# Kernel tuning notes

Hardware: AMD Instinct MI355X
Metric: run time of the kernel (lower is better)

The kernel has to match this reference:

```python
import jax, jax.numpy as jnp
import numpy as np

HEADS = 16
D_MODEL = 1024
D_HEAD = D_MODEL // HEADS


def setup_inputs() -> dict:
    key = jax.random.key(0)
    ks = jax.random.split(key, 12)
    B, S = 4, 2048
    scale = D_MODEL ** -0.5
    inp = {
        "q": jax.random.normal(ks[0], (B, S, D_MODEL), jnp.float32),
        "k": jax.random.normal(ks[1], (B, S, D_MODEL), jnp.float32),
        "v": jax.random.normal(ks[2], (B, S, D_MODEL), jnp.float32),
        # causal mask: True = masked position
        "mask": jnp.triu(jnp.ones((S, S), bool), k=1)[None].repeat(B, axis=0),
        "wq": jax.random.normal(ks[3], (D_MODEL, D_MODEL), jnp.float32) * scale,
        "bq": jnp.zeros((D_MODEL,), jnp.float32),
        "wk": jax.random.normal(ks[4], (D_MODEL, D_MODEL), jnp.float32) * scale,
        "bk": jnp.zeros((D_MODEL,), jnp.float32),
        "wv": jax.random.normal(ks[5], (D_MODEL, D_MODEL), jnp.float32) * scale,
        "bv": jnp.zeros((D_MODEL,), jnp.float32),
        "wo": jax.random.normal(ks[6], (D_MODEL, D_MODEL), jnp.float32) * scale,
        "bo": jnp.zeros((D_MODEL,), jnp.float32),
    }
    return inp


def _split_head(x):
    B, S, _ = x.shape
    return x.reshape(B, S, HEADS, D_HEAD).transpose(0, 2, 1, 3)  # [B,H,S,D]


def reference(q, k, v, mask, wq, bq, wk, bk, wv, bv, wo, bo):
    # linear projections (torch Linear: x @ W^T + b)
    qh = _split_head(q @ wq.T + bq) * (D_HEAD ** -0.5)
    kh = _split_head(k @ wk.T + bk)
    vh = _split_head(v @ wv.T + bv)
    # scores [B,H,Sq,Sk]
    scores = jnp.einsum("bhqd,bhkd->bhqk", qh, kh)
    scores = jnp.where(mask[:, None, :, :], -1e20, scores)
    weights = jax.nn.softmax(scores, axis=-1)  # dropout p=0 in eval
    ctx = jnp.einsum("bhqk,bhkd->bhqd", weights, vh)
    B, H, S, D = ctx.shape
    ctx = ctx.transpose(0, 2, 1, 3).reshape(B, S, H * D)
    return ctx @ wo.T + bo
```

## Files before the change

kernel.cpp:

```cpp
#include <hip/hip_runtime.h>
#include <hip/hip_bf16.h>
#include <cstdint>
#include <cstddef>

typedef unsigned short u16;
typedef unsigned int u32;
using short8  = __attribute__((ext_vector_type(8))) short;
using f32x4   = __attribute__((ext_vector_type(4))) float;
using f32x16  = __attribute__((ext_vector_type(16))) float;
using u32x4   = __attribute__((ext_vector_type(4))) u32;

#define SCALE_Q 0.18033688011112043f

#define WAITVM(N) asm volatile("s_waitcnt vmcnt(" #N ")" ::: "memory")

__device__ inline u16 f2bf(float f) {
  return __builtin_bit_cast(u16, __float2bfloat16(f));
}

__device__ inline u32 cvt_pk_bf16(float a, float b) {
  u32 r;
  asm("v_cvt_pk_bf16_f32 %0, %1, %2" : "=v"(r) : "v"(a), "v"(b));
  return r;
}

__device__ inline f32x4 mfma16(short8 a, short8 b, f32x4 c) {
  return __builtin_amdgcn_mfma_f32_16x16x32_bf16(a, b, c, 0, 0, 0);
}
__device__ inline f32x16 mfma32(short8 a, short8 b, f32x16 c) {
  return __builtin_amdgcn_mfma_f32_32x32x16_bf16(a, b, c, 0, 0, 0);
}

__device__ inline void gload16(const void* g, void* l) {
  __builtin_amdgcn_global_load_lds(
      (const __attribute__((address_space(1))) void*)g,
      (__attribute__((address_space(3))) void*)l,
      16, 0, 0);
}

__global__ __launch_bounds__(256)
void prep(const float* __restrict__ q, const float* __restrict__ k,
          const float* __restrict__ v,
          const float* __restrict__ wq, const float* __restrict__ wk,
          const float* __restrict__ wv, const float* __restrict__ wo,
          u16* __restrict__ Wb, u16* __restrict__ Act) {
  const int c = blockIdx.x * 256 + threadIdx.x;
  const float* src;
  u16* dst;
  float sc = 1.f;
  size_t off;
  if (c < 524288) {
    const int m = c >> 17;
    off = (size_t)(c & 131071) * 8;
    src = (m == 0) ? wq : (m == 1) ? wk : (m == 2) ? wv : wo;
    if (m == 0) sc = SCALE_Q;
    dst = Wb + (size_t)m * 1048576;
  } else {
    const int c2 = c - 524288;
    const int m = c2 >> 20;
    off = (size_t)(c2 & 1048575) * 8;
    src = (m == 0) ? q : (m == 1) ? k : v;
    dst = Act + (size_t)m * 8388608;
  }
  f32x4 a = *(const f32x4*)(src + off);
  f32x4 b = *(const f32x4*)(src + off + 4);
  short8 vv;
#pragma unroll
  for (int j = 0; j < 4; ++j) { vv[j] = (short)f2bf(a[j] * sc); vv[4 + j] = (short)f2bf(b[j] * sc); }
  *(short8*)&dst[off] = vv;
}

struct GemmArgs {
  const u16* Act; const u16* ctx; const u16* Wb;
  const float* bq; const float* bk; const float* bv; const float* bo;
  u16* Qs; u16* Ks; u16* Vs; float* out;
};

__global__ __launch_bounds__(256, 3)
void gemm_proj(GemmArgs ga, int modeBase) {
  const int mode = modeBase + blockIdx.z;
  const int bx = blockIdx.x;
  const int bm = ((bx & 7) << 3) | (bx >> 3);
  const int bn = blockIdx.y;
  const int tid = threadIdx.x;
  const int w = tid >> 6, lane = tid & 63;
  const int wr = w >> 1, wc = w & 1;
  const int l15 = lane & 15, g = lane >> 4;

  const u16* Am = (mode == 3) ? ga.ctx : ga.Act + (size_t)mode * 8388608;
  const u16* Wm = ga.Wb + (size_t)mode * 1048576;
  const float* bias = (mode == 0) ? ga.bq : (mode == 1) ? ga.bk : (mode == 2) ? ga.bv : ga.bo;

  __shared__ u16 As[2][128 * 64];
  __shared__ u16 Bs[2][128 * 64];

  f32x4 acc[4][4] = {};
  const int m0 = bm * 128, n0 = bn * 128;

  const int r_lo = lane >> 3;
  const int sc8 = ((lane & 7) ^ (lane >> 3)) * 8;

  auto stage = [&](int k0, int slot) {
#pragma unroll
    for (int i = 0; i < 4; ++i) {
      const int row = i * 32 + w * 8 + r_lo;
      const int db = i * 2048 + w * 512;
      gload16(Am + (size_t)(m0 + row) * 1024 + k0 + sc8, &As[slot][db]);
      gload16(Wm + (size_t)(n0 + row) * 1024 + k0 + sc8, &Bs[slot][db]);
    }
  };

  auto compute = [&](int slot) {
#pragma unroll
    for (int kk = 0; kk < 2; ++kk) {
      short8 av[4], bv4[4];
#pragma unroll
      for (int mi = 0; mi < 4; ++mi) {
        const int row = wr * 64 + mi * 16 + l15;
        av[mi] = *(const short8*)&As[slot][row * 64 + ((((kk << 2) | g)) ^ (row & 7)) * 8];
      }
#pragma unroll
      for (int ni = 0; ni < 4; ++ni) {
        const int row = wc * 64 + ni * 16 + l15;
        bv4[ni] = *(const short8*)&Bs[slot][row * 64 + ((((kk << 2) | g)) ^ (row & 7)) * 8];
      }
#pragma unroll
      for (int mi = 0; mi < 4; ++mi)
#pragma unroll
        for (int ni = 0; ni < 4; ++ni)
          acc[mi][ni] = mfma16(av[mi], bv4[ni], acc[mi][ni]);
    }
  };

  stage(0, 0);
  stage(64, 1);

#pragma unroll 2
  for (int t = 0; t < 14; ++t) {
    WAITVM(8);
    __builtin_amdgcn_s_barrier();
    __builtin_amdgcn_sched_barrier(0);
    compute(t & 1);
    __builtin_amdgcn_s_barrier();
    __builtin_amdgcn_sched_barrier(0);
    stage((t + 2) * 64, t & 1);
  }
  WAITVM(8);
  __builtin_amdgcn_s_barrier();
  __builtin_amdgcn_sched_barrier(0);
  compute(0);
  WAITVM(0);
  __builtin_amdgcn_s_barrier();
  __builtin_amdgcn_sched_barrier(0);
  compute(1);

  float bvals[4];
#pragma unroll
  for (int ni = 0; ni < 4; ++ni)
    bvals[ni] = bias[n0 + wc * 64 + ni * 16 + l15] * ((mode == 0) ? SCALE_Q : 1.f);

  if (mode == 3) {
#pragma unroll
    for (int mi = 0; mi < 4; ++mi)
#pragma unroll
      for (int ni = 0; ni < 4; ++ni)
#pragma unroll
        for (int r = 0; r < 4; ++r) {
          const int m = m0 + wr * 64 + mi * 16 + g * 4 + r;
          const int n = n0 + wc * 64 + ni * 16 + l15;
          ga.out[(size_t)m * 1024 + n] = acc[mi][ni][r] + bvals[ni];
        }
  } else {
    u16* O = (mode == 0) ? ga.Qs : (mode == 1) ? ga.Ks : ga.Vs;
#pragma unroll
    for (int mi = 0; mi < 4; ++mi)
#pragma unroll
      for (int ni = 0; ni < 4; ++ni)
#pragma unroll
        for (int r = 0; r < 4; ++r) {
          const int m = m0 + wr * 64 + mi * 16 + g * 4 + r;
          const int n = n0 + wc * 64 + ni * 16 + l15;
          const int b = m >> 11, s = m & 2047, hh = n >> 6, d = n & 63;
          const float val = acc[mi][ni][r] + bvals[ni];
          const size_t base = (size_t)(b * 16 + hh) * 131072;
          size_t idx;
          if (mode == 2) {
            const int sp = (s & ~12) | ((s & 4) << 1) | ((s & 8) >> 1);
            const int kt = sp >> 5, w5 = sp & 31;
            const int j = ((d >> 5) << 1) | (w5 >> 4);
            const int hi2 = (w5 >> 3) & 1, e = w5 & 7;
            idx = base + (size_t)kt * 2048 + j * 512 + hi2 * 256 + (d & 31) * 8 + e;
          } else {
            const int s32 = s >> 5, l31 = s & 31;
            const int t2 = d >> 4, hi2 = (d >> 3) & 1, e = d & 7;
            idx = base + (size_t)s32 * 2048 + t2 * 512 + hi2 * 256 + l31 * 8 + e;
          }
          O[idx] = f2bf(val);
        }
  }
}

__global__ __launch_bounds__(256)
void attn_fwd(const u16* __restrict__ Qs, const u16* __restrict__ Ks,
              const u16* __restrict__ Vs, u16* __restrict__ ctx) {
  const int bh = blockIdx.x;
  const int qt = 15 - blockIdx.y;
  const int tid = threadIdx.x;
  const int w = tid >> 6, lane = tid & 63;
  const int l31 = lane & 31, hi = lane >> 5;

  const u16* Qb = Qs + (size_t)bh * 131072;
  const u16* Kb = Ks + (size_t)bh * 131072 + lane * 8;
  const u16* Vb = Vs + (size_t)bh * 131072 + lane * 8;
  const int b = bh >> 4, hh = bh & 15;

  const int qw0 = qt * 128 + w * 32;
  const int nkt = (qw0 >> 5) + 1;
  const int qrow = qw0 + l31;

  short8 qf[4];
  {
    const u16* qp = Qb + (size_t)(qw0 >> 5) * 2048 + lane * 8;
#pragma unroll
    for (int t = 0; t < 4; ++t) qf[t] = *(const short8*)(qp + t * 512);
  }

  f32x16 oacc0 = {}, oacc1 = {};
  float lsum = 0.f;

  auto body = [&](const short8* kf, const short8* vf, int kt, bool last) {
    f32x16 st = {};
    __builtin_amdgcn_s_setprio(1);
    st = mfma32(kf[0], qf[0], st);
    st = mfma32(kf[1], qf[1], st);
    st = mfma32(kf[2], qf[2], st);
    st = mfma32(kf[3], qf[3], st);
    __builtin_amdgcn_s_setprio(0);
    if (last) {
#pragma unroll
      for (int r = 0; r < 16; ++r) {
        const int ka = kt * 32 + (r & 3) + 8 * (r >> 2) + 4 * hi;
        if (ka > qrow) st[r] = -1e30f;
      }
    }
    float p[16];
#pragma unroll
    for (int r = 0; r < 16; ++r) p[r] = __builtin_amdgcn_exp2f(st[r]);
    {
      float s0 = (p[0] + p[1]) + (p[2] + p[3]);
      float s1 = (p[4] + p[5]) + (p[6] + p[7]);
      float s2 = (p[8] + p[9]) + (p[10] + p[11]);
      float s3 = (p[12] + p[13]) + (p[14] + p[15]);
      lsum += (s0 + s1) + (s2 + s3);
    }
    u32x4 a0, a1;
#pragma unroll
    for (int v2 = 0; v2 < 4; ++v2) {
      a0[v2] = cvt_pk_bf16(p[2 * v2], p[2 * v2 + 1]);
      a1[v2] = cvt_pk_bf16(p[8 + 2 * v2], p[9 + 2 * v2]);
    }
    const short8 pb0 = __builtin_bit_cast(short8, a0);
    const short8 pb1 = __builtin_bit_cast(short8, a1);
    __builtin_amdgcn_s_setprio(1);
    oacc0 = mfma32(vf[0], pb0, oacc0);
    oacc0 = mfma32(vf[1], pb1, oacc0);
    oacc1 = mfma32(vf[2], pb0, oacc1);
    oacc1 = mfma32(vf[3], pb1, oacc1);
    __builtin_amdgcn_s_setprio(0);
  };

  short8 kA[4], vA[4], kB[4], vB[4];
#pragma unroll
  for (int t = 0; t < 4; ++t) {
    kA[t] = *(const short8*)(Kb + t * 512);
    vA[t] = *(const short8*)(Vb + t * 512);
  }

  for (int kt = 0; ; ) {
    const bool lastA = (kt + 1 == nkt);
    if (!lastA) {
      const u16* kp = Kb + (size_t)(kt + 1) * 2048;
      const u16* vp = Vb + (size_t)(kt + 1) * 2048;
#pragma unroll
      for (int t = 0; t < 4; ++t) {
        kB[t] = *(const short8*)(kp + t * 512);
        vB[t] = *(const short8*)(vp + t * 512);
      }
    }
    body(kA, vA, kt, lastA);
    if (lastA) break;
    ++kt;
    const bool lastB = (kt + 1 == nkt);
    if (!lastB) {
      const u16* kp = Kb + (size_t)(kt + 1) * 2048;
      const u16* vp = Vb + (size_t)(kt + 1) * 2048;
#pragma unroll
      for (int t = 0; t < 4; ++t) {
        kA[t] = *(const short8*)(kp + t * 512);
        vA[t] = *(const short8*)(vp + t * 512);
      }
    }
    body(kB, vB, kt, lastB);
    if (lastB) break;
    ++kt;
  }

  lsum += __shfl_xor(lsum, 32);
  const float inv = __builtin_amdgcn_rcpf(lsum);

  u16* crow = ctx + ((size_t)(b * 2048 + qrow)) * 1024 + hh * 64;
#pragma unroll
  for (int r = 0; r < 16; r += 2) {
    const int d0 = (r & 3) + 8 * (r >> 2) + 4 * hi;
    *(u32*)&crow[d0]      = cvt_pk_bf16(oacc0[r] * inv, oacc0[r + 1] * inv);
    *(u32*)&crow[32 + d0] = cvt_pk_bf16(oacc1[r] * inv, oacc1[r + 1] * inv);
  }
}

extern "C" void kernel_launch(void* const* d_in, const int* in_sizes, int n_in,
                              void* d_out, int out_size, void* d_ws, size_t ws_size,
                              hipStream_t stream) {
  const float* q  = (const float*)d_in[0];
  const float* k  = (const float*)d_in[1];
  const float* v  = (const float*)d_in[2];
  const float* wq = (const float*)d_in[4];
  const float* bq = (const float*)d_in[5];
  const float* wk = (const float*)d_in[6];
  const float* bk = (const float*)d_in[7];
  const float* wv = (const float*)d_in[8];
  const float* bv = (const float*)d_in[9];
  const float* wo = (const float*)d_in[10];
  const float* bo = (const float*)d_in[11];

  char* ws = (char*)d_ws;
  const size_t WBSZ  = (size_t)4 * 1048576 * sizeof(u16);
  const size_t ACTSZ = (size_t)3 * 8388608 * sizeof(u16);
  const size_t SZ    = (size_t)64 * 131072 * sizeof(u16);
  u16* Wb  = (u16*)(ws);
  u16* Act = (u16*)(ws + WBSZ);
  u16* Qs  = (u16*)(ws + WBSZ + ACTSZ);
  u16* Ks  = (u16*)(ws + WBSZ + ACTSZ + SZ);
  u16* Vs  = (u16*)(ws + WBSZ + ACTSZ + 2 * SZ);
  u16* ctx = (u16*)(ws + WBSZ + ACTSZ + 3 * SZ);

  GemmArgs ga;
  ga.Act = Act; ga.ctx = ctx; ga.Wb = Wb;
  ga.bq = bq; ga.bk = bk; ga.bv = bv; ga.bo = bo;
  ga.Qs = Qs; ga.Ks = Ks; ga.Vs = Vs; ga.out = (float*)d_out;

  prep<<<dim3(14336), dim3(256), 0, stream>>>(q, k, v, wq, wk, wv, wo, Wb, Act);
  gemm_proj<<<dim3(64, 8, 3), dim3(256), 0, stream>>>(ga, 0);
  attn_fwd<<<dim3(64, 16), dim3(256), 0, stream>>>(Qs, Ks, Vs, ctx);
  gemm_proj<<<dim3(64, 8, 1), dim3(256), 0, stream>>>(ga, 3);
}
```

Baseline: 176.2 us.

## Stage K/V tiles cooperatively in double-buffered LDS for attention kernel

Previously each of the four waves in an attention block loaded every K/V tile straight from global memory into its own registers, so each tile was fetched four times per block. Now the waves share the work: each wave fetches a quarter of the tile into a two-slot LDS buffer, with vmcnt waits and block barriers, and the next-but-one tile is prefetched while the current one is used. The cost is that all waves now iterate to the block's maximum tile count, so waves with shorter causal ranges compute fully masked tiles. It also adds two barriers per iteration.

```diff
diff --git a/kernel.cpp b/kernel.cpp
--- a/kernel.cpp
+++ b/kernel.cpp
@@ -210,13 +210,27 @@
   const int l31 = lane & 31, hi = lane >> 5;
 
   const u16* Qb = Qs + (size_t)bh * 131072;
-  const u16* Kb = Ks + (size_t)bh * 131072 + lane * 8;
-  const u16* Vb = Vs + (size_t)bh * 131072 + lane * 8;
+  const u16* Kb = Ks + (size_t)bh * 131072;
+  const u16* Vb = Vs + (size_t)bh * 131072;
   const int b = bh >> 4, hh = bh & 15;
 
   const int qw0 = qt * 128 + w * 32;
-  const int nkt = (qw0 >> 5) + 1;
+  const int nktw = (qw0 >> 5) + 1;
+  const int nktmax = qt * 4 + 4;
   const int qrow = qw0 + l31;
+
+  __shared__ u16 Klds[2][2048];
+  __shared__ u16 Vlds[2][2048];
+
+  auto stageKV = [&](int kt, int slot) {
+    const size_t toff = (size_t)kt * 2048 + (w * 64 + lane) * 8;
+    gload16(Kb + toff, &Klds[slot][w * 512]);
+    gload16(Vb + toff, &Vlds[slot][w * 512]);
+  };
+
+  stageKV(0, 0);
+  stageKV(1, 1);
+  __builtin_amdgcn_sched_barrier(0);
 
   short8 qf[4];
   {
@@ -224,11 +238,24 @@
 #pragma unroll
     for (int t = 0; t < 4; ++t) qf[t] = *(const short8*)(qp + t * 512);
   }
+  __builtin_amdgcn_sched_barrier(0);
 
   f32x16 oacc0 = {}, oacc1 = {};
   float lsum = 0.f;
 
-  auto body = [&](const short8* kf, const short8* vf, int kt, bool last) {
+  for (int kt = 0; kt < nktmax; ++kt) {
+    const int slot = kt & 1;
+    if (kt + 1 < nktmax) { WAITVM(2); } else { WAITVM(0); }
+    __builtin_amdgcn_s_barrier();
+    __builtin_amdgcn_sched_barrier(0);
+
+    short8 kf[4], vf[4];
+#pragma unroll
+    for (int t = 0; t < 4; ++t) {
+      kf[t] = *(const short8*)&Klds[slot][t * 512 + lane * 8];
+      vf[t] = *(const short8*)&Vlds[slot][t * 512 + lane * 8];
+    }
+
     f32x16 st = {};
     __builtin_amdgcn_s_setprio(1);
     st = mfma32(kf[0], qf[0], st);
@@ -236,13 +263,15 @@
     st = mfma32(kf[2], qf[2], st);
     st = mfma32(kf[3], qf[3], st);
     __builtin_amdgcn_s_setprio(0);
-    if (last) {
+
+    if (kt >= nktw - 1) {
 #pragma unroll
       for (int r = 0; r < 16; ++r) {
         const int ka = kt * 32 + (r & 3) + 8 * (r >> 2) + 4 * hi;
         if (ka > qrow) st[r] = -1e30f;
       }
     }
+
     float p[16];
 #pragma unroll
     for (int r = 0; r < 16; ++r) p[r] = __builtin_amdgcn_exp2f(st[r]);
@@ -267,42 +296,10 @@
     oacc1 = mfma32(vf[2], pb0, oacc1);
     oacc1 = mfma32(vf[3], pb1, oacc1);
     __builtin_amdgcn_s_setprio(0);
-  };
-
-  short8 kA[4], vA[4], kB[4], vB[4];
-#pragma unroll
-  for (int t = 0; t < 4; ++t) {
-    kA[t] = *(const short8*)(Kb + t * 512);
-    vA[t] = *(const short8*)(Vb + t * 512);
-  }
-
-  for (int kt = 0; ; ) {
-    const bool lastA = (kt + 1 == nkt);
-    if (!lastA) {
-      const u16* kp = Kb + (size_t)(kt + 1) * 2048;
-      const u16* vp = Vb + (size_t)(kt + 1) * 2048;
-#pragma unroll
-      for (int t = 0; t < 4; ++t) {
-        kB[t] = *(const short8*)(kp + t * 512);
-        vB[t] = *(const short8*)(vp + t * 512);
-      }
-    }
-    body(kA, vA, kt, lastA);
-    if (lastA) break;
-    ++kt;
-    const bool lastB = (kt + 1 == nkt);
-    if (!lastB) {
-      const u16* kp = Kb + (size_t)(kt + 1) * 2048;
-      const u16* vp = Vb + (size_t)(kt + 1) * 2048;
-#pragma unroll
-      for (int t = 0; t < 4; ++t) {
-        kA[t] = *(const short8*)(kp + t * 512);
-        vA[t] = *(const short8*)(vp + t * 512);
-      }
-    }
-    body(kB, vB, kt, lastB);
-    if (lastB) break;
-    ++kt;
+
+    __builtin_amdgcn_s_barrier();
+    __builtin_amdgcn_sched_barrier(0);
+    if (kt + 2 < nktmax) stageKV(kt + 2, slot);
   }
 
   lsum += __shfl_xor(lsum, 32);
```

After: 176.9 us. No clear change (+0.4%).
